# Kernel tuning notes

Measured on AMD Instinct MI355X. Metric: run time of the kernel, lower is better.

Reference implementation:

```python
import jax, jax.numpy as jnp
import numpy as np

B, T, D = 2, 2048, 1024
H = 16
HD = D // H  # 128
L = 8  # latent prefix length
SCALE = HD ** -0.5


def setup_inputs() -> dict:
    key = jax.random.key(0)
    ks = jax.random.split(key, 12)
    p = lambda k, shape: jax.random.normal(k, shape, dtype=jnp.float32) * 0.02
    return {
        "hidden_states": jax.random.normal(ks[0], (B, T, D), dtype=jnp.float32),
        "decoder_latent": jax.random.normal(ks[1], (B, H, L, 2 * HD), dtype=jnp.float32),
        "attention_mask": jnp.zeros((B, 1, T, L + T), dtype=jnp.float32),
        "Wq": p(ks[2], (D, D)), "bq": p(ks[3], (D,)),
        "Wk": p(ks[4], (D, D)), "bk": p(ks[5], (D,)),
        "Wv": p(ks[6], (D, D)), "bv": p(ks[7], (D,)),
        "Wo": p(ks[8], (D, D)), "bo": p(ks[9], (D,)),
    }


def _heads(x):
    # [B, S, D] -> [B, H, S, HD]
    return x.reshape(x.shape[0], x.shape[1], H, HD).transpose(0, 2, 1, 3)


def reference(hidden_states, decoder_latent, attention_mask,
              Wq, bq, Wk, bk, Wv, bv, Wo, bo):
    q = _heads((hidden_states @ Wq + bq) * SCALE)            # [B,H,T,HD]
    k = _heads(hidden_states @ Wk + bk)                      # [B,H,T,HD]
    v = _heads(hidden_states @ Wv + bv)
    lk, lv = jnp.split(decoder_latent, 2, axis=-1)           # [B,H,L,HD] each
    k = jnp.concatenate([lk, k], axis=2)                     # [B,H,L+T,HD]
    v = jnp.concatenate([lv, v], axis=2)
    scores = jnp.einsum('bhtd,bhsd->bhts', q, k) + attention_mask
    probs = jax.nn.softmax(scores, axis=-1)                  # [B,H,T,L+T]
    o = jnp.einsum('bhts,bhsd->bhtd', probs, v)              # [B,H,T,HD]
    o = o.transpose(0, 2, 1, 3).reshape(hidden_states.shape[0], -1, D)
    return o @ Wo + bo
```

## Files before the change

### kernel.cpp

```cpp
#include <hip/hip_runtime.h>

#define T_ 2048
#define D_ 1024
#define H_ 16
#define HD_ 64
#define L_ 8
#define S_ 2056
#define M_ 4096
#define SCALE_ 0.125f

typedef unsigned short u16;
typedef u16 u16x4 __attribute__((ext_vector_type(4)));
typedef u16 u16x8 __attribute__((ext_vector_type(8)));
typedef __bf16 bf16x8 __attribute__((ext_vector_type(8)));
typedef float f32x4 __attribute__((ext_vector_type(4)));

#define MFMA(a, b, c) __builtin_amdgcn_mfma_f32_16x16x32_bf16((a), (b), (c), 0, 0, 0)

__device__ __forceinline__ u16 f2bf(float x) {
    unsigned u = __float_as_uint(x);
    return (u16)((u + 0x7fffu + ((u >> 16) & 1u)) >> 16);
}
__device__ __forceinline__ float bf2f(u16 h) { return __uint_as_float(((unsigned)h) << 16); }
__device__ __forceinline__ bf16x8 ldfrag(const u16* p) {
    u16x8 u = *(const u16x8*)p;
    return __builtin_bit_cast(bf16x8, u);
}
__device__ __forceinline__ void split_store(float v, u16* ph, u16* pl) {
    u16 h = f2bf(v);
    *ph = h;
    *pl = f2bf(v - bf2f(h));
}

__global__ __launch_bounds__(256) void cvt_hidden(const float* __restrict__ hs,
                                                  u16* __restrict__ Hh, u16* __restrict__ Hl) {
    size_t i4 = (size_t)blockIdx.x * 256 + threadIdx.x;
    f32x4 v = ((const f32x4*)hs)[i4];
    u16x4 hi, lo;
#pragma unroll
    for (int j = 0; j < 4; ++j) {
        u16 h = f2bf(v[j]);
        hi[j] = h;
        lo[j] = f2bf(v[j] - bf2f(h));
    }
    ((u16x4*)Hh)[i4] = hi;
    ((u16x4*)Hl)[i4] = lo;
}

__global__ __launch_bounds__(256) void tr_w(const float* __restrict__ Wq, const float* __restrict__ Wk,
                                            const float* __restrict__ Wv, const float* __restrict__ Wo,
                                            u16* __restrict__ WT) {
    const int z = blockIdx.z;
    const float* W = (z == 0) ? Wq : (z == 1) ? Wk : (z == 2) ? Wv : Wo;
    u16* WTh = WT + (size_t)z * 2097152u;
    u16* WTl = WTh + 1048576u;
    __shared__ float t_s[64][68];
    const int k0 = blockIdx.y * 64, n0 = blockIdx.x * 64;
    const int tid = threadIdx.x;
#pragma unroll
    for (int p = 0; p < 4; ++p) {
        int slot = tid + p * 256;
        int kr = slot >> 4, seg = slot & 15;
        *(f32x4*)&t_s[kr][seg * 4] = *(const f32x4*)(W + (size_t)(k0 + kr) * D_ + n0 + seg * 4);
    }
    __syncthreads();
#pragma unroll
    for (int p = 0; p < 4; ++p) {
        int slot = tid + p * 256;
        int nr = slot >> 4, ks = slot & 15;
        u16x4 hi, lo;
#pragma unroll
        for (int j = 0; j < 4; ++j) {
            float v = t_s[ks * 4 + j][nr];
            u16 h = f2bf(v);
            hi[j] = h;
            lo[j] = f2bf(v - bf2f(h));
        }
        size_t o = (size_t)(n0 + nr) * D_ + k0 + ks * 4;
        *(u16x4*)(WTh + o) = hi;
        *(u16x4*)(WTl + o) = lo;
    }
}

__device__ __forceinline__ void gemm_core(const u16* __restrict__ Ah, const u16* __restrict__ Al,
                                          const u16* __restrict__ BTh, const u16* __restrict__ BTl,
                                          int bm, int bn, f32x4 acc[4][4]) {
    __shared__ u16 As[2][128][40];
    __shared__ u16 Bs[2][128][40];
    const int tid = threadIdx.x;
    const int lane = tid & 63, w = tid >> 6;
    const int wm = w >> 1, wn = w & 1;
    const int c = lane & 15, rg = lane >> 4;
    for (int k0 = 0; k0 < D_; k0 += 32) {
        __syncthreads();
#pragma unroll
        for (int i = 0; i < 4; ++i) {
            int slot = tid + i * 256;
            int pl = slot >> 9, r = (slot >> 2) & 127, q = slot & 3;
            *(u16x8*)&As[pl][r][q * 8] =
                *(const u16x8*)((pl ? Al : Ah) + (size_t)(bm * 128 + r) * D_ + k0 + q * 8);
            *(u16x8*)&Bs[pl][r][q * 8] =
                *(const u16x8*)((pl ? BTl : BTh) + (size_t)(bn * 128 + r) * D_ + k0 + q * 8);
        }
        __syncthreads();
        bf16x8 afh[4], afl[4], bfh[4], bfl[4];
#pragma unroll
        for (int mi = 0; mi < 4; ++mi) {
            int rr = wm * 64 + mi * 16 + c;
            afh[mi] = ldfrag(&As[0][rr][8 * rg]);
            afl[mi] = ldfrag(&As[1][rr][8 * rg]);
        }
#pragma unroll
        for (int ni = 0; ni < 4; ++ni) {
            int rr = wn * 64 + ni * 16 + c;
            bfh[ni] = ldfrag(&Bs[0][rr][8 * rg]);
            bfl[ni] = ldfrag(&Bs[1][rr][8 * rg]);
        }
#pragma unroll
        for (int mi = 0; mi < 4; ++mi) {
#pragma unroll
            for (int ni = 0; ni < 4; ++ni) {
                acc[mi][ni] = MFMA(afh[mi], bfh[ni], acc[mi][ni]);
                acc[mi][ni] = MFMA(afh[mi], bfl[ni], acc[mi][ni]);
                acc[mi][ni] = MFMA(afl[mi], bfh[ni], acc[mi][ni]);
            }
        }
    }
}

__global__ __launch_bounds__(256) void gemm_qkv(
    const u16* __restrict__ Ah, const u16* __restrict__ Al, const u16* __restrict__ WT,
    const float* __restrict__ bq, const float* __restrict__ bk, const float* __restrict__ bv,
    u16* __restrict__ Qh, u16* __restrict__ Ql, u16* __restrict__ Kh, u16* __restrict__ Kl,
    u16* __restrict__ Vh, u16* __restrict__ Vl) {
    const int z = blockIdx.z;
    const u16* BTh = WT + (size_t)z * 2097152u;
    const u16* BTl = BTh + 1048576u;
    f32x4 acc[4][4];
    f32x4 zero = {0.f, 0.f, 0.f, 0.f};
#pragma unroll
    for (int a = 0; a < 4; ++a) {
#pragma unroll
        for (int b2 = 0; b2 < 4; ++b2) acc[a][b2] = zero;
    }
    gemm_core(Ah, Al, BTh, BTl, blockIdx.y, blockIdx.x, acc);
    const int lane = threadIdx.x & 63, w = threadIdx.x >> 6;
    const int wm = w >> 1, wn = w & 1, c = lane & 15, rg = lane >> 4;
    const float* bias = (z == 0) ? bq : ((z == 1) ? bk : bv);
#pragma unroll
    for (int ni = 0; ni < 4; ++ni) {
        int n = blockIdx.x * 128 + wn * 64 + ni * 16 + c;
        float bb = bias[n];
        int hh = n >> 6, hd = n & 63;
#pragma unroll
        for (int mi = 0; mi < 4; ++mi) {
#pragma unroll
            for (int r = 0; r < 4; ++r) {
                int m = blockIdx.y * 128 + wm * 64 + mi * 16 + rg * 4 + r;
                int batch = m >> 11, t = m & 2047;
                float val = acc[mi][ni][r] + bb;
                if (z == 0) {
                    val *= SCALE_;
                    size_t o = ((size_t)(batch * H_ + hh) * T_ + t) * HD_ + hd;
                    split_store(val, &Qh[o], &Ql[o]);
                } else {
                    size_t o = ((size_t)(batch * H_ + hh) * S_ + (t + L_)) * HD_ + hd;
                    if (z == 1) split_store(val, &Kh[o], &Kl[o]);
                    else        split_store(val, &Vh[o], &Vl[o]);
                }
            }
        }
    }
}

__global__ __launch_bounds__(256) void latent_fill(const float* __restrict__ lat,
                                                   u16* __restrict__ Kh, u16* __restrict__ Kl,
                                                   u16* __restrict__ Vh, u16* __restrict__ Vl) {
    int i = blockIdx.x * 256 + threadIdx.x;
    float v = lat[i];
    int cc = i & 127, l = (i >> 7) & 7, h = (i >> 10) & 15, b = i >> 14;
    size_t o = ((size_t)(b * H_ + h) * S_ + l) * HD_ + (cc & 63);
    if (cc < 64) split_store(v, &Kh[o], &Kl[o]);
    else         split_store(v, &Vh[o], &Vl[o]);
}

__global__ __launch_bounds__(256) void tr_v(const u16* __restrict__ Vh, const u16* __restrict__ Vl,
                                            u16* __restrict__ VTh, u16* __restrict__ VTl) {
    const int bh = blockIdx.y;
    const int s0 = blockIdx.x * 64;
    const int tid = threadIdx.x;
    __shared__ u16 t_s[64][72];
#pragma unroll
    for (int pl = 0; pl < 2; ++pl) {
        const u16* src = pl ? Vl : Vh;
        u16* dst = pl ? VTl : VTh;
        __syncthreads();
#pragma unroll
        for (int p = 0; p < 2; ++p) {
            int slot = tid + p * 256;
            int sr = slot >> 3, seg = slot & 7;
            int s = s0 + sr;
            u16x8 v = {0, 0, 0, 0, 0, 0, 0, 0};
            if (s < S_) v = *(const u16x8*)(src + ((size_t)bh * S_ + s) * HD_ + seg * 8);
            *(u16x8*)&t_s[sr][seg * 8] = v;
        }
        __syncthreads();
#pragma unroll
        for (int p = 0; p < 2; ++p) {
            int slot = tid + p * 256;
            int hd = slot & 63, sc = slot >> 6;
            if (s0 + sc * 8 < S_) {
                u16x8 v;
#pragma unroll
                for (int j = 0; j < 8; ++j) v[j] = t_s[sc * 8 + j][hd];
                *(u16x8*)(dst + ((size_t)bh * HD_ + hd) * S_ + s0 + sc * 8) = v;
            }
        }
    }
}

__global__ __launch_bounds__(256, 4) void attn(
    const u16* __restrict__ Qh, const u16* __restrict__ Ql,
    const u16* __restrict__ Kh, const u16* __restrict__ Kl,
    const u16* __restrict__ VTh, const u16* __restrict__ VTl,
    const float* __restrict__ mask, u16* __restrict__ Oh, u16* __restrict__ Ol) {
    __shared__ u16 Ks[2][64][64];
    __shared__ u16 Vs[2][64][64];
    __shared__ u16 Ps[4][16][64];
    const int tid = threadIdx.x, lane = tid & 63, w = tid >> 6;
    const int bh = blockIdx.y, b = bh >> 4, h = bh & 15;
    const int t0 = blockIdx.x * 64;
    const int c = lane & 15, rg = lane >> 4;
    const int c7 = c & 7;

    bf16x8 qh[2], ql[2];
    {
        const int t = t0 + w * 16 + c;
        const size_t qbase = ((size_t)bh * T_ + t) * HD_;
#pragma unroll
        for (int ks = 0; ks < 2; ++ks) {
            qh[ks] = ldfrag(Qh + qbase + ks * 32 + 8 * rg);
            ql[ks] = ldfrag(Ql + qbase + ks * 32 + 8 * rg);
        }
    }
    f32x4 oa[4];
    f32x4 zero = {0.f, 0.f, 0.f, 0.f};
#pragma unroll
    for (int f = 0; f < 4; ++f) oa[f] = zero;
    float mrun[4], lrun[4];
#pragma unroll
    for (int r = 0; r < 4; ++r) { mrun[r] = -1e30f; lrun[r] = 0.f; }
    const float* mrow[4];
#pragma unroll
    for (int r = 0; r < 4; ++r)
        mrow[r] = mask + ((size_t)b * T_ + t0 + w * 16 + rg * 4 + r) * S_;

    for (int s0 = 0; s0 < S_; s0 += 64) {
        __syncthreads();
#pragma unroll
        for (int i = 0; i < 4; ++i) {
            int slot = tid + i * 256;
            int pl = slot >> 9, row = (slot >> 3) & 63, seg = slot & 7;
            int s = s0 + row;
            u16x8 v = {0, 0, 0, 0, 0, 0, 0, 0};
            if (s < S_) v = *(const u16x8*)((pl ? Kl : Kh) + ((size_t)bh * S_ + s) * HD_ + seg * 8);
            *(u16x8*)&Ks[pl][row][(seg ^ (row & 7)) * 8] = v;
        }
#pragma unroll
        for (int i = 0; i < 4; ++i) {
            int slot = tid + i * 256;
            int pl = slot >> 9, row = (slot >> 3) & 63, seg = slot & 7;
            int ss = s0 + seg * 8;
            u16x8 v = {0, 0, 0, 0, 0, 0, 0, 0};
            if (ss < S_) v = *(const u16x8*)((pl ? VTl : VTh) + ((size_t)bh * HD_ + row) * S_ + ss);
            *(u16x8*)&Vs[pl][row][(seg ^ (row & 7)) * 8] = v;
        }
        float mreg[4][4];
#pragma unroll
        for (int r = 0; r < 4; ++r) {
#pragma unroll
            for (int cf = 0; cf < 4; ++cf) {
                int sa = s0 + cf * 16 + c;
                mreg[r][cf] = (sa < S_) ? mrow[r][sa] : 0.f;
            }
        }
        __syncthreads();

        f32x4 sc[4];
#pragma unroll
        for (int cf = 0; cf < 4; ++cf) sc[cf] = zero;
#pragma unroll
        for (int ks = 0; ks < 2; ++ks) {
#pragma unroll
            for (int cf = 0; cf < 4; ++cf) {
                int g = ((ks * 4 + rg) ^ c7) * 8;
                bf16x8 kfh = ldfrag(&Ks[0][cf * 16 + c][g]);
                bf16x8 kfl = ldfrag(&Ks[1][cf * 16 + c][g]);
                sc[cf] = MFMA(qh[ks], kfh, sc[cf]);
                sc[cf] = MFMA(ql[ks], kfh, sc[cf]);
                sc[cf] = MFMA(qh[ks], kfl, sc[cf]);
            }
        }
        float tmax[4], tsum[4];
#pragma unroll
        for (int r = 0; r < 4; ++r) {
#pragma unroll
            for (int cf = 0; cf < 4; ++cf) {
                int sa = s0 + cf * 16 + c;
                if (sa < S_) sc[cf][r] += mreg[r][cf];
                else         sc[cf][r] = -1e30f;
            }
            tmax[r] = fmaxf(fmaxf(sc[0][r], sc[1][r]), fmaxf(sc[2][r], sc[3][r]));
        }
#pragma unroll
        for (int mm = 1; mm < 16; mm <<= 1) {
#pragma unroll
            for (int r = 0; r < 4; ++r) tmax[r] = fmaxf(tmax[r], __shfl_xor(tmax[r], mm));
        }
#pragma unroll
        for (int r = 0; r < 4; ++r) {
            float mn = fmaxf(mrun[r], tmax[r]);
            float alpha = __expf(mrun[r] - mn);
            mrun[r] = mn;
#pragma unroll
            for (int cf = 0; cf < 4; ++cf) sc[cf][r] = __expf(sc[cf][r] - mn);
            tsum[r] = (sc[0][r] + sc[1][r]) + (sc[2][r] + sc[3][r]);
            lrun[r] *= alpha;
#pragma unroll
            for (int f = 0; f < 4; ++f) oa[f][r] *= alpha;
        }
#pragma unroll
        for (int mm = 1; mm < 16; mm <<= 1) {
#pragma unroll
            for (int r = 0; r < 4; ++r) tsum[r] += __shfl_xor(tsum[r], mm);
        }
#pragma unroll
        for (int r = 0; r < 4; ++r) lrun[r] += tsum[r];

#pragma unroll
        for (int r = 0; r < 4; ++r) {
            int prow = rg * 4 + r;
#pragma unroll
            for (int cf = 0; cf < 4; ++cf) {
                int pg = (cf * 2 + (c >> 3)) ^ (prow & 7);
                Ps[w][prow][pg * 8 + c7] = f2bf(sc[cf][r]);
            }
        }
#pragma unroll
        for (int kf = 0; kf < 2; ++kf) {
            int g = ((kf * 4 + rg) ^ c7) * 8;
            bf16x8 pa = ldfrag(&Ps[w][c][g]);
#pragma unroll
            for (int f = 0; f < 4; ++f) {
                bf16x8 vh = ldfrag(&Vs[0][f * 16 + c][g]);
                bf16x8 vl = ldfrag(&Vs[1][f * 16 + c][g]);
                oa[f] = MFMA(pa, vh, oa[f]);
                oa[f] = MFMA(pa, vl, oa[f]);
            }
        }
    }
#pragma unroll
    for (int f = 0; f < 4; ++f) {
#pragma unroll
        for (int r = 0; r < 4; ++r) {
            int tg = t0 + w * 16 + rg * 4 + r;
            float val = oa[f][r] / lrun[r];
            int col = h * HD_ + f * 16 + c;
            size_t o = ((size_t)b * T_ + tg) * D_ + col;
            split_store(val, &Oh[o], &Ol[o]);
        }
    }
}

__global__ __launch_bounds__(256) void gemm_fin(
    const u16* __restrict__ Ah, const u16* __restrict__ Al, const u16* __restrict__ BTh_,
    const float* __restrict__ bo, float* __restrict__ out) {
    const u16* BTh = BTh_;
    const u16* BTl = BTh_ + 1048576u;
    f32x4 acc[4][4];
    f32x4 zero = {0.f, 0.f, 0.f, 0.f};
#pragma unroll
    for (int a = 0; a < 4; ++a) {
#pragma unroll
        for (int b2 = 0; b2 < 4; ++b2) acc[a][b2] = zero;
    }
    gemm_core(Ah, Al, BTh, BTl, blockIdx.y, blockIdx.x, acc);
    const int lane = threadIdx.x & 63, w = threadIdx.x >> 6;
    const int wm = w >> 1, wn = w & 1, c = lane & 15, rg = lane >> 4;
#pragma unroll
    for (int ni = 0; ni < 4; ++ni) {
        int n = blockIdx.x * 128 + wn * 64 + ni * 16 + c;
        float bb = bo[n];
#pragma unroll
        for (int mi = 0; mi < 4; ++mi) {
#pragma unroll
            for (int r = 0; r < 4; ++r) {
                int m = blockIdx.y * 128 + wm * 64 + mi * 16 + rg * 4 + r;
                out[(size_t)m * D_ + n] = acc[mi][ni][r] + bb;
            }
        }
    }
}

extern "C" void kernel_launch(void* const* d_in, const int* in_sizes, int n_in,
                              void* d_out, int out_size, void* d_ws, size_t ws_size,
                              hipStream_t stream) {
    (void)in_sizes; (void)n_in; (void)out_size;
    if (ws_size < 100859904ull) return;
    const float* hs  = (const float*)d_in[0];
    const float* lat = (const float*)d_in[1];
    const float* msk = (const float*)d_in[2];
    const float* Wq = (const float*)d_in[3];
    const float* bq = (const float*)d_in[4];
    const float* Wk = (const float*)d_in[5];
    const float* bk = (const float*)d_in[6];
    const float* Wv = (const float*)d_in[7];
    const float* bv = (const float*)d_in[8];
    const float* Wo = (const float*)d_in[9];
    const float* bo = (const float*)d_in[10];
    float* out = (float*)d_out;
    char* ws = (char*)d_ws;

    u16* Hh  = (u16*)(ws + 0ull);
    u16* Hl  = (u16*)(ws + 8388608ull);
    u16* WT  = (u16*)(ws + 16777216ull);
    u16* Qh  = (u16*)(ws + 33554432ull);
    u16* Ql  = (u16*)(ws + 41943040ull);
    u16* Kh  = (u16*)(ws + 50331648ull);
    u16* Kl  = (u16*)(ws + 58753024ull);
    u16* Vh  = (u16*)(ws + 67174400ull);
    u16* Vl  = (u16*)(ws + 75595776ull);
    u16* VTh = (u16*)(ws + 84017152ull);
    u16* VTl = (u16*)(ws + 92438528ull);
    u16* Oh  = Hh;
    u16* Ol  = Hl;

    cvt_hidden<<<4096, 256, 0, stream>>>(hs, Hh, Hl);
    tr_w<<<dim3(16, 16, 4), 256, 0, stream>>>(Wq, Wk, Wv, Wo, WT);
    gemm_qkv<<<dim3(8, 32, 3), 256, 0, stream>>>(Hh, Hl, WT, bq, bk, bv, Qh, Ql, Kh, Kl, Vh, Vl);
    latent_fill<<<128, 256, 0, stream>>>(lat, Kh, Kl, Vh, Vl);
    tr_v<<<dim3(33, 32), 256, 0, stream>>>(Vh, Vl, VTh, VTl);
    attn<<<dim3(32, 32), 256, 0, stream>>>(Qh, Ql, Kh, Kl, VTh, VTl, msk, Oh, Ol);
    gemm_fin<<<dim3(8, 32), 256, 0, stream>>>(Oh, Ol, WT + 3u * 2097152u, bo, out);
}
```

Measured before the change: 488.6 us.

## Drop split-bf16 low terms for V, PV and output projection paths

Computes V projection, the P·V product and the output projection with single bf16 terms instead of the hi/lo split-bf16 three-term scheme, using a new one-term GEMM core. This removes the low-part buffers, their transposes and half of the MFMAs on those paths. K/V tiles in attention are now prefetched into registers for the next iteration, and the occupancy hint goes from 4 to 5. The trade-off is lower numerical precision in V, P·V and the final projection.

```diff
diff --git a/kernel.cpp b/kernel.cpp
--- a/kernel.cpp
+++ b/kernel.cpp
@@ -128,25 +128,54 @@
     }
 }
 
+__device__ __forceinline__ void gemm_core_1t(const u16* __restrict__ Ah, const u16* __restrict__ BTh,
+                                             int bm, int bn, f32x4 acc[4][4]) {
+    __shared__ u16 As1[128][40];
+    __shared__ u16 Bs1[128][40];
+    const int tid = threadIdx.x;
+    const int lane = tid & 63, w = tid >> 6;
+    const int wm = w >> 1, wn = w & 1;
+    const int c = lane & 15, rg = lane >> 4;
+    for (int k0 = 0; k0 < D_; k0 += 32) {
+        __syncthreads();
+#pragma unroll
+        for (int i = 0; i < 2; ++i) {
+            int slot = tid + i * 256;
+            int r = slot >> 2, q = slot & 3;
+            *(u16x8*)&As1[r][q * 8] = *(const u16x8*)(Ah + (size_t)(bm * 128 + r) * D_ + k0 + q * 8);
+            *(u16x8*)&Bs1[r][q * 8] = *(const u16x8*)(BTh + (size_t)(bn * 128 + r) * D_ + k0 + q * 8);
+        }
+        __syncthreads();
+        bf16x8 af[4], bf[4];
+#pragma unroll
+        for (int mi = 0; mi < 4; ++mi) af[mi] = ldfrag(&As1[wm * 64 + mi * 16 + c][8 * rg]);
+#pragma unroll
+        for (int ni = 0; ni < 4; ++ni) bf[ni] = ldfrag(&Bs1[wn * 64 + ni * 16 + c][8 * rg]);
+#pragma unroll
+        for (int mi = 0; mi < 4; ++mi) {
+#pragma unroll
+            for (int ni = 0; ni < 4; ++ni) acc[mi][ni] = MFMA(af[mi], bf[ni], acc[mi][ni]);
+        }
+    }
+}
+
 __global__ __launch_bounds__(256) void gemm_qkv(
     const u16* __restrict__ Ah, const u16* __restrict__ Al, const u16* __restrict__ WT,
-    const float* __restrict__ bq, const float* __restrict__ bk, const float* __restrict__ bv,
-    u16* __restrict__ Qh, u16* __restrict__ Ql, u16* __restrict__ Kh, u16* __restrict__ Kl,
-    u16* __restrict__ Vh, u16* __restrict__ Vl) {
+    const float* __restrict__ bq, const float* __restrict__ bk,
+    u16* __restrict__ Qh, u16* __restrict__ Ql, u16* __restrict__ Kh, u16* __restrict__ Kl) {
     const int z = blockIdx.z;
     const u16* BTh = WT + (size_t)z * 2097152u;
     const u16* BTl = BTh + 1048576u;
     f32x4 acc[4][4];
     f32x4 zero = {0.f, 0.f, 0.f, 0.f};
 #pragma unroll
-    for (int a = 0; a < 4; ++a) {
+    for (int a = 0; a < 4; ++a)
 #pragma unroll
         for (int b2 = 0; b2 < 4; ++b2) acc[a][b2] = zero;
-    }
     gemm_core(Ah, Al, BTh, BTl, blockIdx.y, blockIdx.x, acc);
     const int lane = threadIdx.x & 63, w = threadIdx.x >> 6;
     const int wm = w >> 1, wn = w & 1, c = lane & 15, rg = lane >> 4;
-    const float* bias = (z == 0) ? bq : ((z == 1) ? bk : bv);
+    const float* bias = (z == 0) ? bq : bk;
 #pragma unroll
     for (int ni = 0; ni < 4; ++ni) {
         int n = blockIdx.x * 128 + wn * 64 + ni * 16 + c;
@@ -165,9 +194,38 @@
                     split_store(val, &Qh[o], &Ql[o]);
                 } else {
                     size_t o = ((size_t)(batch * H_ + hh) * S_ + (t + L_)) * HD_ + hd;
-                    if (z == 1) split_store(val, &Kh[o], &Kl[o]);
-                    else        split_store(val, &Vh[o], &Vl[o]);
+                    split_store(val, &Kh[o], &Kl[o]);
                 }
+            }
+        }
+    }
+}
+
+__global__ __launch_bounds__(256) void gemm_v(
+    const u16* __restrict__ Ah, const u16* __restrict__ BTh,
+    const float* __restrict__ bv, u16* __restrict__ Vh) {
+    f32x4 acc[4][4];
+    f32x4 zero = {0.f, 0.f, 0.f, 0.f};
+#pragma unroll
+    for (int a = 0; a < 4; ++a)
+#pragma unroll
+        for (int b2 = 0; b2 < 4; ++b2) acc[a][b2] = zero;
+    gemm_core_1t(Ah, BTh, blockIdx.y, blockIdx.x, acc);
+    const int lane = threadIdx.x & 63, w = threadIdx.x >> 6;
+    const int wm = w >> 1, wn = w & 1, c = lane & 15, rg = lane >> 4;
+#pragma unroll
+    for (int ni = 0; ni < 4; ++ni) {
+        int n = blockIdx.x * 128 + wn * 64 + ni * 16 + c;
+        float bb = bv[n];
+        int hh = n >> 6, hd = n & 63;
+#pragma unroll
+        for (int mi = 0; mi < 4; ++mi) {
+#pragma unroll
+            for (int r = 0; r < 4; ++r) {
+                int m = blockIdx.y * 128 + wm * 64 + mi * 16 + rg * 4 + r;
+                int batch = m >> 11, t = m & 2047;
+                size_t o = ((size_t)(batch * H_ + hh) * S_ + (t + L_)) * HD_ + hd;
+                Vh[o] = f2bf(acc[mi][ni][r] + bb);
             }
         }
     }
@@ -175,57 +233,49 @@
 
 __global__ __launch_bounds__(256) void latent_fill(const float* __restrict__ lat,
                                                    u16* __restrict__ Kh, u16* __restrict__ Kl,
-                                                   u16* __restrict__ Vh, u16* __restrict__ Vl) {
+                                                   u16* __restrict__ Vh) {
     int i = blockIdx.x * 256 + threadIdx.x;
     float v = lat[i];
     int cc = i & 127, l = (i >> 7) & 7, h = (i >> 10) & 15, b = i >> 14;
     size_t o = ((size_t)(b * H_ + h) * S_ + l) * HD_ + (cc & 63);
     if (cc < 64) split_store(v, &Kh[o], &Kl[o]);
-    else         split_store(v, &Vh[o], &Vl[o]);
-}
-
-__global__ __launch_bounds__(256) void tr_v(const u16* __restrict__ Vh, const u16* __restrict__ Vl,
-                                            u16* __restrict__ VTh, u16* __restrict__ VTl) {
+    else         Vh[o] = f2bf(v);
+}
+
+__global__ __launch_bounds__(256) void tr_v(const u16* __restrict__ Vh, u16* __restrict__ VTh) {
     const int bh = blockIdx.y;
     const int s0 = blockIdx.x * 64;
     const int tid = threadIdx.x;
     __shared__ u16 t_s[64][72];
 #pragma unroll
-    for (int pl = 0; pl < 2; ++pl) {
-        const u16* src = pl ? Vl : Vh;
-        u16* dst = pl ? VTl : VTh;
-        __syncthreads();
-#pragma unroll
-        for (int p = 0; p < 2; ++p) {
-            int slot = tid + p * 256;
-            int sr = slot >> 3, seg = slot & 7;
-            int s = s0 + sr;
-            u16x8 v = {0, 0, 0, 0, 0, 0, 0, 0};
-            if (s < S_) v = *(const u16x8*)(src + ((size_t)bh * S_ + s) * HD_ + seg * 8);
-            *(u16x8*)&t_s[sr][seg * 8] = v;
-        }
-        __syncthreads();
-#pragma unroll
-        for (int p = 0; p < 2; ++p) {
-            int slot = tid + p * 256;
-            int hd = slot & 63, sc = slot >> 6;
-            if (s0 + sc * 8 < S_) {
-                u16x8 v;
-#pragma unroll
-                for (int j = 0; j < 8; ++j) v[j] = t_s[sc * 8 + j][hd];
-                *(u16x8*)(dst + ((size_t)bh * HD_ + hd) * S_ + s0 + sc * 8) = v;
-            }
-        }
-    }
-}
-
-__global__ __launch_bounds__(256, 4) void attn(
+    for (int p = 0; p < 2; ++p) {
+        int slot = tid + p * 256;
+        int sr = slot >> 3, seg = slot & 7;
+        int s = s0 + sr;
+        u16x8 v = {0, 0, 0, 0, 0, 0, 0, 0};
+        if (s < S_) v = *(const u16x8*)(Vh + ((size_t)bh * S_ + s) * HD_ + seg * 8);
+        *(u16x8*)&t_s[sr][seg * 8] = v;
+    }
+    __syncthreads();
+#pragma unroll
+    for (int p = 0; p < 2; ++p) {
+        int slot = tid + p * 256;
+        int hd = slot & 63, sc = slot >> 6;
+        if (s0 + sc * 8 < S_) {
+            u16x8 v;
+#pragma unroll
+            for (int j = 0; j < 8; ++j) v[j] = t_s[sc * 8 + j][hd];
+            *(u16x8*)(VTh + ((size_t)bh * HD_ + hd) * S_ + s0 + sc * 8) = v;
+        }
+    }
+}
+
+__global__ __launch_bounds__(256, 5) void attn(
     const u16* __restrict__ Qh, const u16* __restrict__ Ql,
     const u16* __restrict__ Kh, const u16* __restrict__ Kl,
-    const u16* __restrict__ VTh, const u16* __restrict__ VTl,
-    const float* __restrict__ mask, u16* __restrict__ Oh, u16* __restrict__ Ol) {
+    const u16* __restrict__ VTh, const float* __restrict__ mask, u16* __restrict__ Oh) {
     __shared__ u16 Ks[2][64][64];
-    __shared__ u16 Vs[2][64][64];
+    __shared__ u16 Vs[64][64];
     __shared__ u16 Ps[4][16][64];
     const int tid = threadIdx.x, lane = tid & 63, w = tid >> 6;
     const int bh = blockIdx.y, b = bh >> 4, h = bh & 15;
@@ -255,8 +305,8 @@
     for (int r = 0; r < 4; ++r)
         mrow[r] = mask + ((size_t)b * T_ + t0 + w * 16 + rg * 4 + r) * S_;
 
-    for (int s0 = 0; s0 < S_; s0 += 64) {
-        __syncthreads();
+    u16x8 kreg[4], vreg[2];
+    auto LOADT = [&](int s0) {
 #pragma unroll
         for (int i = 0; i < 4; ++i) {
             int slot = tid + i * 256;
@@ -264,16 +314,33 @@
             int s = s0 + row;
             u16x8 v = {0, 0, 0, 0, 0, 0, 0, 0};
             if (s < S_) v = *(const u16x8*)((pl ? Kl : Kh) + ((size_t)bh * S_ + s) * HD_ + seg * 8);
-            *(u16x8*)&Ks[pl][row][(seg ^ (row & 7)) * 8] = v;
-        }
+            kreg[i] = v;
+        }
+#pragma unroll
+        for (int i = 0; i < 2; ++i) {
+            int slot = tid + i * 256;
+            int row = (slot >> 3) & 63, seg = slot & 7;
+            int ss = s0 + seg * 8;
+            u16x8 v = {0, 0, 0, 0, 0, 0, 0, 0};
+            if (ss < S_) v = *(const u16x8*)(VTh + ((size_t)bh * HD_ + row) * S_ + ss);
+            vreg[i] = v;
+        }
+    };
+    LOADT(0);
+
+    for (int s0 = 0; s0 < S_; s0 += 64) {
+        __syncthreads();
 #pragma unroll
         for (int i = 0; i < 4; ++i) {
             int slot = tid + i * 256;
             int pl = slot >> 9, row = (slot >> 3) & 63, seg = slot & 7;
-            int ss = s0 + seg * 8;
-            u16x8 v = {0, 0, 0, 0, 0, 0, 0, 0};
-            if (ss < S_) v = *(const u16x8*)((pl ? VTl : VTh) + ((size_t)bh * HD_ + row) * S_ + ss);
-            *(u16x8*)&Vs[pl][row][(seg ^ (row & 7)) * 8] = v;
+            *(u16x8*)&Ks[pl][row][(seg ^ (row & 7)) * 8] = kreg[i];
+        }
+#pragma unroll
+        for (int i = 0; i < 2; ++i) {
+            int slot = tid + i * 256;
+            int row = (slot >> 3) & 63, seg = slot & 7;
+            *(u16x8*)&Vs[row][(seg ^ (row & 7)) * 8] = vreg[i];
         }
         float mreg[4][4];
 #pragma unroll
@@ -285,6 +352,7 @@
             }
         }
         __syncthreads();
+        if (s0 + 64 < S_) LOADT(s0 + 64);
 
         f32x4 sc[4];
 #pragma unroll
@@ -352,10 +420,8 @@
             bf16x8 pa = ldfrag(&Ps[w][c][g]);
 #pragma unroll
             for (int f = 0; f < 4; ++f) {
-                bf16x8 vh = ldfrag(&Vs[0][f * 16 + c][g]);
-                bf16x8 vl = ldfrag(&Vs[1][f * 16 + c][g]);
+                bf16x8 vh = ldfrag(&Vs[f * 16 + c][g]);
                 oa[f] = MFMA(pa, vh, oa[f]);
-                oa[f] = MFMA(pa, vl, oa[f]);
             }
         }
     }
@@ -366,25 +432,21 @@
             int tg = t0 + w * 16 + rg * 4 + r;
             float val = oa[f][r] / lrun[r];
             int col = h * HD_ + f * 16 + c;
-            size_t o = ((size_t)b * T_ + tg) * D_ + col;
-            split_store(val, &Oh[o], &Ol[o]);
+            Oh[((size_t)b * T_ + tg) * D_ + col] = f2bf(val);
         }
     }
 }
 
 __global__ __launch_bounds__(256) void gemm_fin(
-    const u16* __restrict__ Ah, const u16* __restrict__ Al, const u16* __restrict__ BTh_,
+    const u16* __restrict__ Ah, const u16* __restrict__ BTh,
     const float* __restrict__ bo, float* __restrict__ out) {
-    const u16* BTh = BTh_;
-    const u16* BTl = BTh_ + 1048576u;
     f32x4 acc[4][4];
     f32x4 zero = {0.f, 0.f, 0.f, 0.f};
 #pragma unroll
-    for (int a = 0; a < 4; ++a) {
+    for (int a = 0; a < 4; ++a)
 #pragma unroll
         for (int b2 = 0; b2 < 4; ++b2) acc[a][b2] = zero;
-    }
-    gemm_core(Ah, Al, BTh, BTl, blockIdx.y, blockIdx.x, acc);
+    gemm_core_1t(Ah, BTh, blockIdx.y, blockIdx.x, acc);
     const int lane = threadIdx.x & 63, w = threadIdx.x >> 6;
     const int wm = w >> 1, wn = w & 1, c = lane & 15, rg = lane >> 4;
 #pragma unroll
@@ -406,7 +468,7 @@
                               void* d_out, int out_size, void* d_ws, size_t ws_size,
                               hipStream_t stream) {
     (void)in_sizes; (void)n_in; (void)out_size;
-    if (ws_size < 100859904ull) return;
+    if (ws_size < 84017152ull) return;
     const float* hs  = (const float*)d_in[0];
     const float* lat = (const float*)d_in[1];
     const float* msk = (const float*)d_in[2];
@@ -429,17 +491,15 @@
     u16* Kh  = (u16*)(ws + 50331648ull);
     u16* Kl  = (u16*)(ws + 58753024ull);
     u16* Vh  = (u16*)(ws + 67174400ull);
-    u16* Vl  = (u16*)(ws + 75595776ull);
-    u16* VTh = (u16*)(ws + 84017152ull);
-    u16* VTl = (u16*)(ws + 92438528ull);
+    u16* VTh = (u16*)(ws + 75595776ull);
     u16* Oh  = Hh;
-    u16* Ol  = Hl;
 
     cvt_hidden<<<4096, 256, 0, stream>>>(hs, Hh, Hl);
     tr_w<<<dim3(16, 16, 4), 256, 0, stream>>>(Wq, Wk, Wv, Wo, WT);
-    gemm_qkv<<<dim3(8, 32, 3), 256, 0, stream>>>(Hh, Hl, WT, bq, bk, bv, Qh, Ql, Kh, Kl, Vh, Vl);
-    latent_fill<<<128, 256, 0, stream>>>(lat, Kh, Kl, Vh, Vl);
-    tr_v<<<dim3(33, 32), 256, 0, stream>>>(Vh, Vl, VTh, VTl);
-    attn<<<dim3(32, 32), 256, 0, stream>>>(Qh, Ql, Kh, Kl, VTh, VTl, msk, Oh, Ol);
-    gemm_fin<<<dim3(8, 32), 256, 0, stream>>>(Oh, Ol, WT + 3u * 2097152u, bo, out);
-}
+    gemm_qkv<<<dim3(8, 32, 2), 256, 0, stream>>>(Hh, Hl, WT, bq, bk, Qh, Ql, Kh, Kl);
+    gemm_v<<<dim3(8, 32), 256, 0, stream>>>(Hh, WT + 2u * 2097152u, bv, Vh);
+    latent_fill<<<128, 256, 0, stream>>>(lat, Kh, Kl, Vh);
+    tr_v<<<dim3(33, 32), 256, 0, stream>>>(Vh, VTh);
+    attn<<<dim3(32, 32), 256, 0, stream>>>(Qh, Ql, Kh, Kl, VTh, msk, Oh);
+    gemm_fin<<<dim3(8, 32), 256, 0, stream>>>(Oh, WT + 3u * 2097152u, bo, out);
+}
```

Measured after the change: 874.7 us. 1.79x slower.
